# Kernel tuning notes

Hardware: AMD Instinct MI355X
Metric: run time of the kernel (lower is better)

## Reference

```python
import jax, jax.numpy as jnp
import numpy as np

B, CIN, H, W = 256, 1280, 7, 7
A, NCLS, HID, NGT = 9, 20, 128, 40
OUT_DIM = 5 * A + NCLS  # 65


def setup_inputs() -> dict:
    key = jax.random.key(0)
    ks = jax.random.split(key, 8)
    features = jax.random.normal(ks[0], (B, CIN, H, W), jnp.float32)
    # grid: (x, y) centers of each feature cell, in feature-map coordinates
    grid = jax.random.uniform(ks[1], (B, H, W, 2), jnp.float32) * 7.0
    # GT boxes (x1, y1, x2, y2, class), padded count NGT per image
    xy1 = jax.random.uniform(ks[2], (B, NGT, 2), jnp.float32) * 5.0
    wh = jax.random.uniform(ks[3], (B, NGT, 2), jnp.float32) * 2.0 + 0.5
    cls = jax.random.randint(ks[4], (B, NGT, 1), 0, NCLS).astype(jnp.float32)
    bboxes = jnp.concatenate([xy1, xy1 + wh, cls], axis=-1)
    # anchor shapes (w, h) as in SingleStageDetector.__init__
    anc = jnp.array([[1.0, 1], [2, 2], [3, 3], [4, 4], [5, 5],
                     [2, 3], [3, 2], [3, 5], [5, 3]], jnp.float32)
    W1 = jax.random.normal(ks[5], (HID, CIN), jnp.float32) * 0.02
    b1 = jnp.zeros((HID,), jnp.float32)
    W2 = jax.random.normal(ks[6], (OUT_DIM, HID), jnp.float32) * 0.02
    b2 = jnp.zeros((OUT_DIM,), jnp.float32)
    return dict(features=features, grid=grid, bboxes=bboxes, anc=anc,
                W1=W1, b1=b1, W2=W2, b2=b2)


def reference(features, grid, bboxes, anc, W1, b1, W2, b2):
    Bx = features.shape[0]
    # --- PredictionNetwork (inference mode; dropout is identity at eval) ---
    h = jnp.einsum('bchw,oc->bohw', features, W1) + b1[None, :, None, None]
    h = jax.nn.leaky_relu(h, negative_slope=0.01)
    out = jnp.einsum('bchw,oc->bohw', h, W2) + b2[None, :, None, None]
    conf_scores = jax.nn.sigmoid(out[:, 4 * A:5 * A])          # (B, A, H, W)
    offsets = out[:, :4 * A].reshape(Bx, A, 4, H, W)
    offsets = jnp.concatenate(
        [jax.nn.sigmoid(offsets[:, :, :2]) - 0.5, offsets[:, :, 2:]], axis=2)
    class_scores = out[:, 5 * A:]                               # (B, C, H, W)
    # --- GenerateAnchor: (B, A, H, W, 4) as (x_tl, y_tl, x_br, y_br) ---
    ctr = grid[:, None]                    # (B, 1, H, W, 2)
    half = anc[None, :, None, None, :] / 2  # (1, A, 1, 1, 2)
    anchors = jnp.concatenate([ctr - half, ctr + half], axis=-1)
    # --- IoU: (B, A*H*W, N) ---
    P = anchors.reshape(Bx, -1, 4)          # (B, AHW, 4)
    gt = bboxes[..., :4]                    # (B, N, 4)
    tl = jnp.maximum(P[:, :, None, :2], gt[:, None, :, :2])
    br = jnp.minimum(P[:, :, None, 2:], gt[:, None, :, 2:])
    inter = jnp.prod(jnp.clip(br - tl, 0.0), axis=-1)  # (B, AHW, N)
    # torch code zeroes intersections for proposals with any coord <= 0
    legal = (jnp.min(P, axis=-1) > 0)[..., None]
    inter = inter * legal
    p_area = ((P[:, :, 2] - P[:, :, 0]) * (P[:, :, 3] - P[:, :, 1]))[:, :, None]
    g_area = ((gt[:, :, 2] - gt[:, :, 0]) * (gt[:, :, 3] - gt[:, :, 1]))[:, None, :]
    iou_mat = inter / (g_area + p_area - inter)
    return (conf_scores, offsets, class_scores, iou_mat)
```

## Files before the change

kernel.cpp:

```cpp
#include <hip/hip_runtime.h>


#define CIN_  1280
#define HW_   49
#define HID_  128
#define OUTD_ 65
#define NGT_  40
#define NP_   441

#define CONF_OFF 0
#define OFFS_OFF 112896
#define CLS_OFF  564480
#define IOU_OFF  815360

#define WS_W1F_U32 81920u
#define WS_W2F_U32 5120u
#define FB_OFF     87040u

typedef __bf16 bf16x8 __attribute__((ext_vector_type(8)));
typedef float  f32x4  __attribute__((ext_vector_type(4)));

__device__ __forceinline__ unsigned pack2bf(float lo, float hi) {
    unsigned short a = __builtin_bit_cast(unsigned short, (__bf16)lo);
    unsigned short b = __builtin_bit_cast(unsigned short, (__bf16)hi);
    return (unsigned)a | ((unsigned)b << 16);
}
__device__ __forceinline__ float sigmoidf_(float v) { return 1.f / (1.f + __expf(-v)); }

__device__ __forceinline__ bf16x8 ld_frag(const unsigned* p) {
    union { uint4 u; bf16x8 v; } x;
    x.u = *(const uint4*)p;
    return x.v;
}
__device__ __forceinline__ bf16x8 as_bf(uint4 u) {
    union { uint4 u; bf16x8 v; } x; x.u = u; return x.v;
}

__global__ __launch_bounds__(256) void prep(
    const float* __restrict__ F,
    const float* __restrict__ W1, const float* __restrict__ W2,
    unsigned* __restrict__ ws)
{
    if (blockIdx.x < 10240) {
        int X = blockIdx.x * 256 + threadIdx.x;
        int lane = X & 63, t = X >> 6;
        int ct = t & 3, bk = t >> 2;
        int k32 = bk % 40, b = bk / 40;
        int quad = lane >> 4, m16 = lane & 15;
        int col = ct * 16 + m16; if (col > 48) col = 48;
        const float* p = F + b * (CIN_ * HW_) + (k32 * 32 + quad * 8) * 49 + col;
        uint4 q;
        q.x = pack2bf(p[0],   p[49]);
        q.y = pack2bf(p[98],  p[147]);
        q.z = pack2bf(p[196], p[245]);
        q.w = pack2bf(p[294], p[343]);
        ((uint4*)(ws + FB_OFF))[X] = q;
        return;
    }
    int X = (blockIdx.x - 10240) * 256 + threadIdx.x;
    if (X < (int)WS_W1F_U32) {
        int sub = X & 3, lane = (X >> 2) & 63, f = X >> 8;
        int mt = f & 7, K32 = f >> 3;
        int o = mt * 16 + (lane & 15);
        int c = K32 * 32 + (lane >> 4) * 8 + sub * 2;
        float2 v = *(const float2*)(W1 + o * CIN_ + c);
        ws[X] = pack2bf(v.x, v.y);
    } else {
        int Y = X - (int)WS_W1F_U32;
        int sub = Y & 3, lane = (Y >> 2) & 63, f = Y >> 8;
        int mt2 = f % 5, ks2 = f / 5;
        int o2 = mt2 * 16 + (lane & 15);
        int c = ks2 * 32 + (lane >> 4) * 8 + sub * 2;
        unsigned val = 0;
        if (o2 < OUTD_) {
            float2 v = *(const float2*)(W2 + o2 * HID_ + c);
            val = pack2bf(v.x, v.y);
        }
        ws[WS_W1F_U32 + Y] = val;
    }
}

__global__ __launch_bounds__(1024, 4) void fused_main(
    const float* __restrict__ grd,
    const float* __restrict__ bbox,
    const float* __restrict__ anc,
    const unsigned* __restrict__ wsW,
    const float* __restrict__ B1,
    const float* __restrict__ B2,
    float* __restrict__ out)
{
    __shared__ __align__(16) unsigned smHT[64 * 68];

    const int tid  = threadIdx.x;
    const int b    = blockIdx.x;
    const int lane = tid & 63;
    const int w    = tid >> 6;
    const int wo   = w >> 1;
    const int ch2  = w & 1;
    const int quad = lane >> 4;
    const int m16  = lane & 15;

    const uint4* Ap = (const uint4*)wsW + wo * 64 + lane;
    const uint4* Fp = (const uint4*)(wsW + FB_OFF) + b * 10240 + ch2 * 128 + lane;
    #define LD_A(k)    Ap[(k) * 512]
    #define LD_B(k, j) Fp[(k) * 256 + (j) * 64]

    f32x4 acc[2] = {(f32x4)(0.f), (f32x4)(0.f)};
    uint4 ar[3], br[3][2];
    #pragma unroll
    for (int d = 0; d < 3; ++d) {
        ar[d] = LD_A(d);
        br[d][0] = LD_B(d, 0);
        br[d][1] = LD_B(d, 1);
    }
    #pragma unroll
    for (int k = 0; k < 40; ++k) {
        const int s = k % 3;
        bf16x8 A = as_bf(ar[s]);
        acc[0] = __builtin_amdgcn_mfma_f32_16x16x32_bf16(A, as_bf(br[s][0]), acc[0], 0, 0, 0);
        acc[1] = __builtin_amdgcn_mfma_f32_16x16x32_bf16(A, as_bf(br[s][1]), acc[1], 0, 0, 0);
        const int kp = (k + 3 < 40) ? k + 3 : 39;
        ar[s] = LD_A(kp);
        br[s][0] = LD_B(kp, 0);
        br[s][1] = LD_B(kp, 1);
    }

    #pragma unroll
    for (int j = 0; j < 2; ++j) {
        int col = (ch2 * 2 + j) * 16 + m16;
        #pragma unroll
        for (int rp = 0; rp < 2; ++rp) {
            int o0 = wo * 16 + quad * 4 + 2 * rp;
            float v0 = acc[j][2 * rp]     + B1[o0];
            float v1 = acc[j][2 * rp + 1] + B1[o0 + 1];
            v0 = v0 > 0.f ? v0 : 0.01f * v0;
            v1 = v1 > 0.f ? v1 : 0.01f * v1;
            smHT[col * 68 + (o0 >> 1)] = pack2bf(v0, v1);
        }
    }
    __syncthreads();

    for (int T = w; T < 20; T += 16) {
        int m2 = T % 5, nt2 = T / 5;
        const uint4* A2p = (const uint4*)(wsW + WS_W1F_U32) + m2 * 64 + lane;
        uint4 a20 = A2p[0], a21 = A2p[320], a22 = A2p[640], a23 = A2p[960];
        f32x4 c2 = (f32x4)(0.f);
        const unsigned* Bb = smHT + (nt2 * 16 + m16) * 68 + quad * 4;
        c2 = __builtin_amdgcn_mfma_f32_16x16x32_bf16(as_bf(a20), ld_frag(Bb +  0), c2, 0, 0, 0);
        c2 = __builtin_amdgcn_mfma_f32_16x16x32_bf16(as_bf(a21), ld_frag(Bb + 16), c2, 0, 0, 0);
        c2 = __builtin_amdgcn_mfma_f32_16x16x32_bf16(as_bf(a22), ld_frag(Bb + 32), c2, 0, 0, 0);
        c2 = __builtin_amdgcn_mfma_f32_16x16x32_bf16(as_bf(a23), ld_frag(Bb + 48), c2, 0, 0, 0);
        int hw = nt2 * 16 + m16;
        if (hw < HW_) {
            #pragma unroll
            for (int r = 0; r < 4; ++r) {
                int o2 = m2 * 16 + quad * 4 + r;
                if (o2 >= OUTD_) continue;
                float aa = c2[r] + B2[o2];
                unsigned dst; float val;
                if (o2 < 36) {
                    int an9 = o2 >> 2, kk = o2 & 3;
                    val = (kk < 2) ? (sigmoidf_(aa) - 0.5f) : aa;
                    dst = OFFS_OFF + b * 1764 + an9 * 196 + kk * 49 + hw;
                } else if (o2 < 45) {
                    val = sigmoidf_(aa);
                    dst = CONF_OFF + b * 441 + (o2 - 36) * 49 + hw;
                } else {
                    val = aa;
                    dst = CLS_OFF + b * 980 + (o2 - 45) * 49 + hw;
                }
                out[dst] = val;
            }
        }
    }

    {
        int gl = (lane < NGT_) ? lane : 0;
        const float* gb = bbox + b * 200 + gl * 5;
        float gx1 = gb[0], gy1 = gb[1], gx2 = gb[2], gy2 = gb[3];
        float gA = (gx2 - gx1) * (gy2 - gy1);
        #pragma unroll 4
        for (int p = w; p < NP_; p += 16) {
            int a9 = p / 49, r = p - a9 * 49;
            float2 ct = *(const float2*)(grd + b * 98 + 2 * r);
            float hx = anc[2 * a9] * 0.5f,  hy = anc[2 * a9 + 1] * 0.5f;
            float px1 = ct.x - hx, py1 = ct.y - hy, px2 = ct.x + hx, py2 = ct.y + hy;
            float pA = (px2 - px1) * (py2 - py1);
            float legal = (fminf(fminf(px1, py1), fminf(px2, py2)) > 0.f) ? 1.f : 0.f;
            float tlx = fmaxf(px1, gx1), tly = fmaxf(py1, gy1);
            float brx = fminf(px2, gx2), bry = fminf(py2, gy2);
            float dx = fmaxf(brx - tlx, 0.f), dy = fmaxf(bry - tly, 0.f);
            float inter = dx * dy * legal;
            float iou = __fdividef(inter, gA + pA - inter);
            if (lane < NGT_)
                out[IOU_OFF + b * (NP_ * NGT_) + p * 40 + lane] = iou;
        }
    }
}

extern "C" void kernel_launch(void* const* d_in, const int* in_sizes, int n_in,
                              void* d_out, int out_size, void* d_ws, size_t ws_size,
                              hipStream_t stream) {
    const float* F  = (const float*)d_in[0];
    const float* G  = (const float*)d_in[1];
    const float* BB = (const float*)d_in[2];
    const float* AN = (const float*)d_in[3];
    const float* W1 = (const float*)d_in[4];
    const float* B1 = (const float*)d_in[5];
    const float* W2 = (const float*)d_in[6];
    const float* B2 = (const float*)d_in[7];
    float* out = (float*)d_out;
    unsigned* wsu = (unsigned*)d_ws;

    prep<<<10580, 256, 0, stream>>>(F, W1, W2, wsu);
    fused_main<<<256, 1024, 0, stream>>>(G, BB, AN, wsu, B1, B2, out);
}
```

Before: 141.9 us.

## Stage feature slab through LDS in prep and split main kernel per half image

The prep kernel now loads each 32-channel feature slab with coalesced float4 reads into shared memory and builds the bf16 MFMA fragments from LDS, replacing scattered strided global reads. The main kernel goes from 256 blocks of 1024 threads to 512 blocks of 512 threads, each block covering half of an image's spatial columns and half of its IoU rows. The GEMM prefetch depth rises from 3 to 4 stages. This is meant to improve global-load coalescing and spread work over more CUs, at the cost of each half-image block reloading the full W1 fragments.

After: 142.4 us. No clear change (+0.4%).

```diff
diff --git a/kernel.cpp b/kernel.cpp
--- a/kernel.cpp
+++ b/kernel.cpp
@@ -36,28 +36,44 @@
     union { uint4 u; bf16x8 v; } x; x.u = u; return x.v;
 }
 
-__global__ __launch_bounds__(256) void prep(
+__global__ __launch_bounds__(128) void prep(
     const float* __restrict__ F,
     const float* __restrict__ W1, const float* __restrict__ W2,
     unsigned* __restrict__ ws)
 {
     if (blockIdx.x < 10240) {
-        int X = blockIdx.x * 256 + threadIdx.x;
-        int lane = X & 63, t = X >> 6;
-        int ct = t & 3, bk = t >> 2;
-        int k32 = bk % 40, b = bk / 40;
-        int quad = lane >> 4, m16 = lane & 15;
-        int col = ct * 16 + m16; if (col > 48) col = 48;
-        const float* p = F + b * (CIN_ * HW_) + (k32 * 32 + quad * 8) * 49 + col;
-        uint4 q;
-        q.x = pack2bf(p[0],   p[49]);
-        q.y = pack2bf(p[98],  p[147]);
-        q.z = pack2bf(p[196], p[245]);
-        q.w = pack2bf(p[294], p[343]);
-        ((uint4*)(ws + FB_OFF))[X] = q;
+        __shared__ __align__(16) float lds[1568];
+        const int X   = blockIdx.x;
+        const int b   = X / 40;
+        const int k32 = X - b * 40;
+        const int tid = threadIdx.x;
+
+        const float4* src = (const float4*)(F + b * (CIN_ * HW_) + k32 * 1568);
+        float4* dst4 = (float4*)lds;
+        dst4[tid]       = src[tid];
+        dst4[tid + 128] = src[tid + 128];
+        dst4[tid + 256] = src[tid + 256];
+        if (tid < 8) dst4[tid + 384] = src[tid + 384];
+        __syncthreads();
+
+        uint4* dst = (uint4*)(ws + FB_OFF) + (unsigned)X * 256;
+        #pragma unroll
+        for (int h2 = 0; h2 < 2; ++h2) {
+            int idx  = h2 * 128 + tid;
+            int ct   = idx >> 6, lane = idx & 63;
+            int quad = lane >> 4, m16 = lane & 15;
+            int col  = ct * 16 + m16; if (col > 48) col = 48;
+            const float* p = lds + quad * 8 * 49 + col;
+            uint4 q;
+            q.x = pack2bf(p[0],   p[49]);
+            q.y = pack2bf(p[98],  p[147]);
+            q.z = pack2bf(p[196], p[245]);
+            q.w = pack2bf(p[294], p[343]);
+            dst[idx] = q;
+        }
         return;
     }
-    int X = (blockIdx.x - 10240) * 256 + threadIdx.x;
+    int X = (blockIdx.x - 10240) * 128 + threadIdx.x;
     if (X < (int)WS_W1F_U32) {
         int sub = X & 3, lane = (X >> 2) & 63, f = X >> 8;
         int mt = f & 7, K32 = f >> 3;
@@ -80,7 +96,7 @@
     }
 }
 
-__global__ __launch_bounds__(1024, 4) void fused_main(
+__global__ __launch_bounds__(512, 4) void fused_main(
     const float* __restrict__ grd,
     const float* __restrict__ bbox,
     const float* __restrict__ anc,
@@ -89,58 +105,56 @@
     const float* __restrict__ B2,
     float* __restrict__ out)
 {
-    __shared__ __align__(16) unsigned smHT[64 * 68];
+    __shared__ __align__(16) unsigned smHT[32 * 68];
 
     const int tid  = threadIdx.x;
-    const int b    = blockIdx.x;
+    const int id   = blockIdx.x;
+    const int b    = id >> 1;
+    const int half = id & 1;
     const int lane = tid & 63;
     const int w    = tid >> 6;
-    const int wo   = w >> 1;
-    const int ch2  = w & 1;
     const int quad = lane >> 4;
     const int m16  = lane & 15;
 
-    const uint4* Ap = (const uint4*)wsW + wo * 64 + lane;
-    const uint4* Fp = (const uint4*)(wsW + FB_OFF) + b * 10240 + ch2 * 128 + lane;
-    #define LD_A(k)    Ap[(k) * 512]
-    #define LD_B(k, j) Fp[(k) * 256 + (j) * 64]
+    const uint4* Ap = (const uint4*)wsW + w * 64 + lane;
+    const uint4* Fp = (const uint4*)(wsW + FB_OFF) + b * 10240 + half * 128 + lane;
 
     f32x4 acc[2] = {(f32x4)(0.f), (f32x4)(0.f)};
-    uint4 ar[3], br[3][2];
+    uint4 ar[4], br[4][2];
     #pragma unroll
-    for (int d = 0; d < 3; ++d) {
-        ar[d] = LD_A(d);
-        br[d][0] = LD_B(d, 0);
-        br[d][1] = LD_B(d, 1);
+    for (int d = 0; d < 4; ++d) {
+        ar[d]    = Ap[d * 512];
+        br[d][0] = Fp[d * 256];
+        br[d][1] = Fp[d * 256 + 64];
     }
     #pragma unroll
     for (int k = 0; k < 40; ++k) {
-        const int s = k % 3;
+        const int s = k & 3;
         bf16x8 A = as_bf(ar[s]);
         acc[0] = __builtin_amdgcn_mfma_f32_16x16x32_bf16(A, as_bf(br[s][0]), acc[0], 0, 0, 0);
         acc[1] = __builtin_amdgcn_mfma_f32_16x16x32_bf16(A, as_bf(br[s][1]), acc[1], 0, 0, 0);
-        const int kp = (k + 3 < 40) ? k + 3 : 39;
-        ar[s] = LD_A(kp);
-        br[s][0] = LD_B(kp, 0);
-        br[s][1] = LD_B(kp, 1);
+        const int kp = (k + 4 < 40) ? k + 4 : 39;
+        ar[s]    = Ap[kp * 512];
+        br[s][0] = Fp[kp * 256];
+        br[s][1] = Fp[kp * 256 + 64];
     }
 
     #pragma unroll
     for (int j = 0; j < 2; ++j) {
-        int col = (ch2 * 2 + j) * 16 + m16;
+        int colL = j * 16 + m16;
         #pragma unroll
         for (int rp = 0; rp < 2; ++rp) {
-            int o0 = wo * 16 + quad * 4 + 2 * rp;
+            int o0 = w * 16 + quad * 4 + 2 * rp;
             float v0 = acc[j][2 * rp]     + B1[o0];
             float v1 = acc[j][2 * rp + 1] + B1[o0 + 1];
             v0 = v0 > 0.f ? v0 : 0.01f * v0;
             v1 = v1 > 0.f ? v1 : 0.01f * v1;
-            smHT[col * 68 + (o0 >> 1)] = pack2bf(v0, v1);
+            smHT[colL * 68 + (o0 >> 1)] = pack2bf(v0, v1);
         }
     }
     __syncthreads();
 
-    for (int T = w; T < 20; T += 16) {
+    for (int T = w; T < 10; T += 8) {
         int m2 = T % 5, nt2 = T / 5;
         const uint4* A2p = (const uint4*)(wsW + WS_W1F_U32) + m2 * 64 + lane;
         uint4 a20 = A2p[0], a21 = A2p[320], a22 = A2p[640], a23 = A2p[960];
@@ -150,7 +164,7 @@
         c2 = __builtin_amdgcn_mfma_f32_16x16x32_bf16(as_bf(a21), ld_frag(Bb + 16), c2, 0, 0, 0);
         c2 = __builtin_amdgcn_mfma_f32_16x16x32_bf16(as_bf(a22), ld_frag(Bb + 32), c2, 0, 0, 0);
         c2 = __builtin_amdgcn_mfma_f32_16x16x32_bf16(as_bf(a23), ld_frag(Bb + 48), c2, 0, 0, 0);
-        int hw = nt2 * 16 + m16;
+        int hw = half * 32 + nt2 * 16 + m16;
         if (hw < HW_) {
             #pragma unroll
             for (int r = 0; r < 4; ++r) {
@@ -179,8 +193,10 @@
         const float* gb = bbox + b * 200 + gl * 5;
         float gx1 = gb[0], gy1 = gb[1], gx2 = gb[2], gy2 = gb[3];
         float gA = (gx2 - gx1) * (gy2 - gy1);
+        const int pstart = half ? 221 : 0;
+        const int pend   = half ? NP_ : 221;
         #pragma unroll 4
-        for (int p = w; p < NP_; p += 16) {
+        for (int p = pstart + w; p < pend; p += 8) {
             int a9 = p / 49, r = p - a9 * 49;
             float2 ct = *(const float2*)(grd + b * 98 + 2 * r);
             float hx = anc[2 * a9] * 0.5f,  hy = anc[2 * a9 + 1] * 0.5f;
@@ -212,6 +228,6 @@
     float* out = (float*)d_out;
     unsigned* wsu = (unsigned*)d_ws;
 
-    prep<<<10580, 256, 0, stream>>>(F, W1, W2, wsu);
-    fused_main<<<256, 1024, 0, stream>>>(G, BB, AN, wsu, B1, B2, out);
-}
+    prep<<<10920, 128, 0, stream>>>(F, W1, W2, wsu);
+    fused_main<<<512, 512, 0, stream>>>(G, BB, AN, wsu, B1, B2, out);
+}
```
